# Kernel optimization log

Hardware: AMD Instinct MI355X
Metric: run time of the kernel (lower is better)

Reference implementation:

```python
import jax, jax.numpy as jnp
import numpy as np

N = 2048      # nodes
E = 65536     # edges (avg degree 32)
IN_C = 512
OUT_C = 512
KP1 = 3       # K=2 Chebyshev -> 3 terms


def setup_inputs() -> dict:
    key = jax.random.key(0)
    k0, k1, k2, k3, k4 = jax.random.split(key, 5)
    X_real = jax.random.normal(k0, (N, IN_C), jnp.float32)
    X_imag = jax.random.normal(k1, (N, IN_C), jnp.float32)
    edges = jax.random.randint(k2, (2, E), 0, N).astype(jnp.int64)
    edge_weight = jax.random.uniform(k3, (E,), jnp.float32)
    q = jnp.float32(0.25)
    stdv = 1.0 / np.sqrt(OUT_C)
    weight = jax.random.uniform(k4, (KP1, IN_C, OUT_C), jnp.float32, -stdv, stdv)
    bias = jnp.zeros((1, OUT_C), jnp.float32)
    return {"X_real": X_real, "X_imag": X_imag, "edges": edges, "q": q,
            "edge_weight": edge_weight, "weight": weight, "bias": bias}


def _cheb_laplacians(edges, edge_weight, q):
    """QinDirect_hermitian_decomp_sparse (norm=True, laplacian=True, max_eigen=2,
    gcn_appr=False) followed by cheb_poly_sparse with K=2. Returns stacked
    real/imag parts of [T0, T1, T2], each [KP1, N, N]."""
    f, e = edges[0], edges[1]
    A = jnp.zeros((N, N), jnp.float32).at[f, e].add(edge_weight)
    A_sym = 0.5 * (A + A.T)
    deg = A_sym.sum(axis=0)
    dinv = jnp.where(deg == 0.0, 1.0, deg) ** -0.5
    A_norm = dinv[:, None] * A_sym * dinv[None, :]   # D^-1/2 A_sym D^-1/2
    theta = (2.0 * jnp.pi) * q * (A - A.T)           # phase matrix
    # L = I - exp(i*theta) .* A_norm ; scaled (2/max_eigen)*L - I with max_eigen=2
    # => L_scaled = -exp(i*theta) .* A_norm
    L1_re = -jnp.cos(theta) * A_norm
    L1_im = -jnp.sin(theta) * A_norm
    eye = jnp.eye(N, dtype=jnp.float32)
    # T2 = 2*L1@L1 - I (complex square in real arithmetic)
    L2_re = 2.0 * (L1_re @ L1_re - L1_im @ L1_im) - eye
    L2_im = 2.0 * (L1_re @ L1_im + L1_im @ L1_re)
    L_re = jnp.stack([eye, L1_re, L2_re])                        # [KP1,N,N]
    L_im = jnp.stack([jnp.zeros((N, N), jnp.float32), L1_im, L2_im])
    return L_re, L_im


def reference(X_real, X_imag, edges, q, edge_weight, weight, bias):
    L_re, L_im = _cheb_laplacians(edges, edge_weight, q)
    # NOTE: original forward swaps the lists: L_norm_real = L_img, L_norm_imag = L_real.
    mr, mi = L_im, L_re
    # per term k: real_k = (mr_k@Xr - mi_k@Xi) @ W_k ; imag_k = (mi_k@Xr + mr_k@Xi) @ W_k
    Ar = jnp.einsum('knm,mf->knf', mr, X_real) - jnp.einsum('knm,mf->knf', mi, X_imag)
    Ai = jnp.einsum('knm,mf->knf', mi, X_real) + jnp.einsum('knm,mf->knf', mr, X_imag)
    real = jnp.einsum('knf,kfo->no', Ar, weight)   # sum over K terms
    imag = jnp.einsum('knf,kfo->no', Ai, weight)
    return real + bias, imag + bias
```

## Files before the change

### kernel.cpp

```cpp
#include <hip/hip_runtime.h>
#include <hip/hip_bf16.h>
#include <math.h>

#define NN 2048
#define CC 512
#define NEDGE 65536

typedef __hip_bfloat16 bf16;
typedef __attribute__((ext_vector_type(8))) short short8;
typedef __attribute__((ext_vector_type(4))) float floatx4;
typedef __attribute__((ext_vector_type(2))) float floatx2;
typedef __attribute__((ext_vector_type(4))) unsigned short us4;
typedef __attribute__((ext_vector_type(2))) unsigned short us2;

static constexpr float TWO_PI_F = 6.2831853071795864769f;

__device__ __forceinline__ unsigned short f2bu(float f) {
    bf16 h = __float2bfloat16(f);
    return *reinterpret_cast<unsigned short*>(&h);
}
__device__ __forceinline__ float bu2f(unsigned short u) {
    return __uint_as_float(((unsigned)u) << 16);
}
__device__ __forceinline__ int get_isbf(const void* qp) {
    return ((((const unsigned*)qp)[0] & 0xFFFFu) == 0x3E80u) ? 1 : 0;
}

__device__ __forceinline__ void gld16(const void* g, void* l) {
    __builtin_amdgcn_global_load_lds(
        (const __attribute__((address_space(1))) unsigned int*)(unsigned long long)(uintptr_t)g,
        (__attribute__((address_space(3))) unsigned int*)(unsigned long long)(uintptr_t)l,
        16, 0, 0);
}

__global__ __launch_bounds__(256) void prep_k(
    const void* __restrict__ xr, const void* __restrict__ xi,
    const void* __restrict__ edges, const void* __restrict__ qp,
    const void* __restrict__ ew, const void* __restrict__ Wt,
    int2* __restrict__ bucket, int* __restrict__ bcnt,
    bf16* __restrict__ Af, bf16* __restrict__ WTo, void* __restrict__ Xc)
{
    int bid = blockIdx.x, t = threadIdx.x;
    int isbf = get_isbf(qp);

    if (bid < 2048) {
        int r = bid;
        float fr0, fr1, fi0, fi1;
        if (isbf) {
            us2 vr = *(const us2*)((const bf16*)xr + (size_t)r * CC + 2 * t);
            us2 vi = *(const us2*)((const bf16*)xi + (size_t)r * CC + 2 * t);
            fr0 = bu2f(vr.x); fr1 = bu2f(vr.y); fi0 = bu2f(vi.x); fi1 = bu2f(vi.y);
        } else {
            floatx2 vr = *(const floatx2*)((const float*)xr + (size_t)r * CC + 2 * t);
            floatx2 vi = *(const floatx2*)((const float*)xi + (size_t)r * CC + 2 * t);
            fr0 = vr.x; fr1 = vr.y; fi0 = vi.x; fi1 = vi.y;
        }
        *(us2*)(Af + (size_t)r * 1536 + 2 * t)        = (us2){f2bu(-fi0), f2bu(-fi1)};
        *(us2*)(Af + (size_t)(NN + r) * 1536 + 2 * t) = (us2){f2bu(fr0), f2bu(fr1)};
        if (isbf)
            ((us4*)Xc)[(size_t)r * 256 + t] = (us4){f2bu(fr0), f2bu(fr1), f2bu(fi0), f2bu(fi1)};
        else
            ((floatx4*)Xc)[(size_t)r * 256 + t] = (floatx4){fr0, fr1, fi0, fi1};
    } else if (bid < 2816) {
        __shared__ float t1[32][33];
        int bw = bid - 2048;
        int k0 = (bw % 48) * 32, o0 = (bw / 48) * 32;
        int tx = t & 31, ty = t >> 5;
#pragma unroll
        for (int rr = 0; rr < 32; rr += 8) {
            size_t sidx = (size_t)(k0 + ty + rr) * CC + o0 + tx;
            t1[ty + rr][tx] = isbf ? __bfloat162float(((const bf16*)Wt)[sidx])
                                   : ((const float*)Wt)[sidx];
        }
        __syncthreads();
#pragma unroll
        for (int rr = 0; rr < 32; rr += 8)
            WTo[(size_t)(o0 + ty + rr) * 1536 + k0 + tx] = __float2bfloat16(t1[tx][ty + rr]);
    } else {
        __shared__ int s_i64;
        if (t < 64) {
            unsigned w0 = ((const unsigned*)edges)[2 * t + 1];
            unsigned w1 = ((const unsigned*)edges)[128 + 2 * t + 1];
            unsigned long long b = __ballot((w0 | w1) != 0u);
            if (t == 0) s_i64 = (b == 0ull) ? 1 : 0;
        }
        __syncthreads();
        int i64 = s_i64;
        int e = (bid - 2816) * 256 + t;
        int f, to;
        if (i64) {
            f  = (int)((const long long*)edges)[e];
            to = (int)((const long long*)edges)[NEDGE + e];
        } else {
            f  = ((const int*)edges)[e];
            to = ((const int*)edges)[NEDGE + e];
        }
        float wv = isbf ? __bfloat162float(((const bf16*)ew)[e]) : ((const float*)ew)[e];
        f &= (NN - 1); to &= (NN - 1);
        int wi = __float_as_int(wv);
        int s0 = atomicAdd(&bcnt[f], 1);
        if (s0 < 256) bucket[(size_t)f * 256 + s0] = make_int2(to, wi);
        int s1 = atomicAdd(&bcnt[to], 1);
        if (s1 < 256) bucket[(size_t)to * 256 + s1] = make_int2(f | 4096, wi);
    }
}

__global__ __launch_bounds__(256) void compact_k(
    const int2* __restrict__ bucket, const int* __restrict__ bcnt,
    float* __restrict__ dinv, int* __restrict__ ecol,
    floatx2* __restrict__ em, int* __restrict__ ecnt)
{
    __shared__ int      idx[NN];
    __shared__ unsigned pres[64];
    __shared__ int      pref[64];
    __shared__ float    s_s[256], s_d[256], red[256];
    __shared__ int      s_n;
    int i = blockIdx.x, t = threadIdx.x;

#pragma unroll
    for (int k = 0; k < NN / 256; ++k) idx[k * 256 + t] = -1;
    if (t < 64) pres[t] = 0u;
    s_s[t] = 0.f; s_d[t] = 0.f;
    __syncthreads();

    int cnt = bcnt[i]; if (cnt > 256) cnt = 256;
    int col = 0, dir = 0; float w = 0.f;
    if (t < cnt) {
        int2 e = bucket[(size_t)i * 256 + t];
        col = e.x & (NN - 1); dir = (e.x >> 12) & 1;
        w = __int_as_float(e.y);
    }
    red[t] = (t < cnt) ? w : 0.f;
    __syncthreads();
    for (int off = 128; off > 0; off >>= 1) {
        if (t < off) red[t] += red[t + off];
        __syncthreads();
    }
    if (t == 0) {
        float d = 0.5f * red[0];
        if (d == 0.f) d = 1.f;
        dinv[i] = rsqrtf(d);
    }
    if (t < cnt) atomicCAS(&idx[col], -1, t);
    __syncthreads();
    bool winner = (t < cnt) && (idx[col] == t);
    if (winner) atomicOr(&pres[col >> 5], 1u << (col & 31));
    __syncthreads();
    if (t == 0) {
        int run = 0;
        for (int wd = 0; wd < 64; ++wd) { pref[wd] = run; run += __popc(pres[wd]); }
        s_n = run;
        ecnt[i] = run;
    }
    __syncthreads();
    if (winner) {
        int slot = pref[col >> 5] + __popc(pres[col >> 5] & ((1u << (col & 31)) - 1u));
        idx[col] = slot;
        ecol[i * 256 + slot] = col;
    }
    __syncthreads();
    if (t < cnt) {
        int sl = idx[col];
        atomicAdd(&s_s[sl], w);
        atomicAdd(&s_d[sl], dir ? -w : w);
    }
    __syncthreads();
    if (t < s_n)
        em[i * 256 + t] = (floatx2){s_s[t], s_d[t]};
}

template<int EPI>
__global__ __launch_bounds__(256) void spmm_k(
    const int* __restrict__ ecol, const floatx2* __restrict__ em,
    const int* __restrict__ ecnt, const float* __restrict__ dinv,
    const void* __restrict__ qp,
    const void* __restrict__ xr, const void* __restrict__ xi,
    const void* __restrict__ Xc, const bf16* __restrict__ Z1in,
    bf16* __restrict__ Z1out, bf16* __restrict__ Af)
{
    int i = blockIdx.x, t = threadIdx.x;
    int isbf = get_isbf(qp);
    int n = ecnt[i];
    __shared__ int   sc[256];
    __shared__ float sre[256], sim[256];
    if (t < n) {
        float qv = isbf ? __bfloat162float(((const bf16*)qp)[0]) : ((const float*)qp)[0];
        int j = ecol[i * 256 + t];
        floatx2 sd = em[i * 256 + t];
        float an = dinv[i] * (0.5f * sd.x) * dinv[j];
        float th = TWO_PI_F * qv * sd.y;
        float sn, cs;
        sincosf(th, &sn, &cs);
        sc[t] = j; sre[t] = -cs * an; sim[t] = sn * an;
    }
    __syncthreads();
    float ar0 = 0.f, ar1 = 0.f, ai0 = 0.f, ai1 = 0.f;

    if (EPI == 1 && !isbf) {
        const floatx4* X4 = (const floatx4*)Xc;
#pragma unroll 4
        for (int s = 0; s < n; ++s) {
            int j = sc[s];
            float re = sre[s], im = sim[s];
            floatx4 v = X4[(((unsigned)j) << 8) + t];
            ar0 += re * v.x - im * v.z;  ai0 += re * v.z + im * v.x;
            ar1 += re * v.y - im * v.w;  ai1 += re * v.w + im * v.y;
        }
    } else {
        const us4* X4 = (const us4*)(EPI == 1 ? Xc : (const void*)Z1in);
#pragma unroll 4
        for (int s = 0; s < n; ++s) {
            int j = sc[s];
            float re = sre[s], im = sim[s];
            us4 v = X4[(((unsigned)j) << 8) + t];
            float vr0 = bu2f(v.x), vr1 = bu2f(v.y);
            float vi0 = bu2f(v.z), vi1 = bu2f(v.w);
            ar0 += re * vr0 - im * vi0;  ai0 += re * vi0 + im * vr0;
            ar1 += re * vr1 - im * vi1;  ai1 += re * vi1 + im * vr1;
        }
    }

    if (EPI == 1) {
        *(us4*)(Z1out + (size_t)i * 1024 + 4 * t) =
            (us4){f2bu(ar0), f2bu(ar1), f2bu(ai0), f2bu(ai1)};
        *(us2*)(Af + (size_t)i * 1536 + 512 + 2 * t)        = (us2){f2bu(-ai0), f2bu(-ai1)};
        *(us2*)(Af + (size_t)(NN + i) * 1536 + 512 + 2 * t) = (us2){f2bu(ar0), f2bu(ar1)};
    } else {
        float xr0, xr1, xi0, xi1;
        if (isbf) {
            us2 vr = *(const us2*)((const bf16*)xr + (size_t)i * CC + 2 * t);
            us2 vi = *(const us2*)((const bf16*)xi + (size_t)i * CC + 2 * t);
            xr0 = bu2f(vr.x); xr1 = bu2f(vr.y); xi0 = bu2f(vi.x); xi1 = bu2f(vi.y);
        } else {
            floatx2 vr = *(const floatx2*)((const float*)xr + (size_t)i * CC + 2 * t);
            floatx2 vi = *(const floatx2*)((const float*)xi + (size_t)i * CC + 2 * t);
            xr0 = vr.x; xr1 = vr.y; xi0 = vi.x; xi1 = vi.y;
        }
        float vre0 = 2.f * ar0 - xr0, vre1 = 2.f * ar1 - xr1;
        float vim0 = 2.f * ai0 - xi0, vim1 = 2.f * ai1 - xi1;
        *(us2*)(Af + (size_t)(NN + i) * 1536 + 1024 + 2 * t) = (us2){f2bu(vre0), f2bu(vre1)};
        *(us2*)(Af + (size_t)i * 1536 + 1024 + 2 * t)        = (us2){f2bu(-vim0), f2bu(-vim1)};
    }
}

__global__ void epi3_k(const bf16* __restrict__ Pb, const void* __restrict__ bias,
                       void* __restrict__ out, const void* __restrict__ qp) {
    int idx = blockIdx.x * 256 + threadIdx.x;
    if (idx >= 4096 * CC) return;
    int isbf = get_isbf(qp);
    int c = idx & (CC - 1);
    float s = 0.f;
#pragma unroll
    for (int z = 0; z < 4; ++z)
        s += __bfloat162float(Pb[(size_t)z * 4096 * CC + idx]);
    float bb = isbf ? __bfloat162float(((const bf16*)bias)[c]) : ((const float*)bias)[c];
    float o = s + bb;
    if (isbf) ((bf16*)out)[idx] = __float2bfloat16(o);
    else      ((float*)out)[idx] = o;
}

__global__ __launch_bounds__(256) void gemm_sk_k(
    const bf16* __restrict__ Ab, const bf16* __restrict__ BTb,
    int M, int N, int K, int klen,
    bf16* __restrict__ Pb)
{
    __shared__ bf16 sA[128 * 64];
    __shared__ bf16 sB[128 * 64];
    int tid = threadIdx.x;
    int w = tid >> 6, lane = tid & 63;
    int row0 = blockIdx.y * 128, col0 = blockIdx.x * 128;
    int kbase = blockIdx.z * klen;
    int wave_m = (w >> 1) * 64, wave_n = (w & 1) * 64;
    int lm = lane & 15, lq = lane >> 4;

    int srow = lane >> 3;
    int sg   = lane & 7;
    int scol = (sg ^ srow) * 8;
    const bf16 *gA[4], *gB[4];
    bf16 *lA[4], *lB[4];
#pragma unroll
    for (int i = 0; i < 4; ++i) {
        int c = w * 4 + i;
        int row = c * 8 + srow;
        gA[i] = Ab  + (size_t)(row0 + row) * K + kbase + scol;
        gB[i] = BTb + (size_t)(col0 + row) * K + kbase + scol;
        lA[i] = sA + c * 512 + lane * 8;
        lB[i] = sB + c * 512 + lane * 8;
    }

    floatx4 acc[4][4];
#pragma unroll
    for (int mf = 0; mf < 4; ++mf)
#pragma unroll
        for (int nf = 0; nf < 4; ++nf)
            acc[mf][nf] = (floatx4){0.f, 0.f, 0.f, 0.f};

    for (int kk = 0; kk < klen; kk += 64) {
        __syncthreads();
#pragma unroll
        for (int i = 0; i < 4; ++i) {
            gld16(gA[i] + kk, lA[i]);
            gld16(gB[i] + kk, lB[i]);
        }
        __syncthreads();
#pragma unroll
        for (int ks = 0; ks < 2; ++ks) {
            short8 af[4], bfv[4];
#pragma unroll
            for (int mf = 0; mf < 4; ++mf) {
                int row = wave_m + mf * 16 + lm;
                int g = (ks * 4 + lq) ^ (row & 7);
                af[mf] = *(const short8*)&sA[row * 64 + g * 8];
            }
#pragma unroll
            for (int nf = 0; nf < 4; ++nf) {
                int row = wave_n + nf * 16 + lm;
                int g = (ks * 4 + lq) ^ (row & 7);
                bfv[nf] = *(const short8*)&sB[row * 64 + g * 8];
            }
#pragma unroll
            for (int mf = 0; mf < 4; ++mf)
#pragma unroll
                for (int nf = 0; nf < 4; ++nf)
                    acc[mf][nf] = __builtin_amdgcn_mfma_f32_16x16x32_bf16(
                        af[mf], bfv[nf], acc[mf][nf], 0, 0, 0);
        }
    }

    bf16* slice = Pb + (size_t)blockIdx.z * M * N;
#pragma unroll
    for (int mf = 0; mf < 4; ++mf) {
#pragma unroll
        for (int nf = 0; nf < 4; ++nf) {
            int gcol = col0 + wave_n + nf * 16 + lm;
#pragma unroll
            for (int r = 0; r < 4; ++r) {
                int grow = row0 + wave_m + mf * 16 + lq * 4 + r;
                slice[(size_t)grow * N + gcol] = __float2bfloat16(acc[mf][nf][r]);
            }
        }
    }
}


extern "C" void kernel_launch(void* const* d_in, const int* in_sizes, int n_in,
                              void* d_out, int out_size, void* d_ws, size_t ws_size,
                              hipStream_t stream) {
    const void* Xr_in = d_in[0];
    const void* Xi_in = d_in[1];
    const void* edges = d_in[2];
    const void* q     = d_in[3];
    const void* ew    = d_in[4];
    const void* Wt    = d_in[5];
    const void* bias  = d_in[6];

    char* base = (char*)d_ws;
    const size_t MB = 1024 * 1024;
    int2*    bucket = (int2*)(base);
    int*     bcnt   = (int*)(base + 8 * MB);
    void*    Xc     = (void*)(base + 12 * MB);
    bf16*    Af     = (bf16*)(base + 32 * MB);
    bf16*    WT     = (bf16*)(base + 44 * MB);
    bf16*    Z1c    = (bf16*)(base + 46 * MB);
    float*   dinv   = (float*)(base + 54 * MB);
    int*     ecnt   = (int*)(base + 54 * MB + 16 * 1024);
    int*     ecol   = (int*)(base + 56 * MB);
    floatx2* em     = (floatx2*)(base + 58 * MB);
    bf16*    Pb     = (bf16*)(base + 56 * MB);

    hipMemsetAsync(bcnt, 0, NN * sizeof(int), stream);

    prep_k<<<3072, 256, 0, stream>>>(Xr_in, Xi_in, edges, q, ew, Wt,
                                     bucket, bcnt, Af, WT, Xc);
    compact_k<<<NN, 256, 0, stream>>>(bucket, bcnt, dinv, ecol, em, ecnt);

    spmm_k<1><<<NN, 256, 0, stream>>>(ecol, em, ecnt, dinv, q, Xr_in, Xi_in,
                                      Xc, nullptr, Z1c, Af);
    spmm_k<2><<<NN, 256, 0, stream>>>(ecol, em, ecnt, dinv, q, Xr_in, Xi_in,
                                      nullptr, Z1c, nullptr, Af);

    gemm_sk_k<<<dim3(CC / 128, 4096 / 128, 4), 256, 0, stream>>>(
        Af, WT, 4096, CC, 1536, 384, Pb);
    epi3_k<<<(4096 * CC) / 256, 256, 0, stream>>>(Pb, bias, d_out, q);
}
```

Before: 172.2 us.

## Regroup prep kernels, vectorize epilogue, raise spmm unroll and occupancy hint

Edge scattering moves into its own small kernel. Compaction is merged with the X and W conversion work into a single mid kernel that uses a shared-memory union, so the launch count stays the same but the grouping changes. The final reduction epilogue now handles four outputs per thread with vector loads and stores. The spmm kernel gets a launch_bounds occupancy hint and unroll 8 on its gather loop, which could raise register pressure or cause spills.

```diff
diff --git a/kernel.cpp b/kernel.cpp
--- a/kernel.cpp
+++ b/kernel.cpp
@@ -33,18 +33,116 @@
         16, 0, 0);
 }
 
-__global__ __launch_bounds__(256) void prep_k(
+__global__ __launch_bounds__(256) void scat_k(
+    const void* __restrict__ edges, const void* __restrict__ qp,
+    const void* __restrict__ ew,
+    int2* __restrict__ bucket, int* __restrict__ bcnt)
+{
+    __shared__ int s_i64;
+    int t = threadIdx.x;
+    int isbf = get_isbf(qp);
+    if (t < 64) {
+        unsigned w0 = ((const unsigned*)edges)[2 * t + 1];
+        unsigned w1 = ((const unsigned*)edges)[128 + 2 * t + 1];
+        unsigned long long b = __ballot((w0 | w1) != 0u);
+        if (t == 0) s_i64 = (b == 0ull) ? 1 : 0;
+    }
+    __syncthreads();
+    int i64 = s_i64;
+    int e = blockIdx.x * 256 + t;
+    int f, to;
+    if (i64) {
+        f  = (int)((const long long*)edges)[e];
+        to = (int)((const long long*)edges)[NEDGE + e];
+    } else {
+        f  = ((const int*)edges)[e];
+        to = ((const int*)edges)[NEDGE + e];
+    }
+    float wv = isbf ? __bfloat162float(((const bf16*)ew)[e]) : ((const float*)ew)[e];
+    f &= (NN - 1); to &= (NN - 1);
+    int wi = __float_as_int(wv);
+    int s0 = atomicAdd(&bcnt[f], 1);
+    if (s0 < 256) bucket[(size_t)f * 256 + s0] = make_int2(to, wi);
+    int s1 = atomicAdd(&bcnt[to], 1);
+    if (s1 < 256) bucket[(size_t)to * 256 + s1] = make_int2(f | 4096, wi);
+}
+
+__global__ __launch_bounds__(256) void mid_k(
+    const int2* __restrict__ bucket, const int* __restrict__ bcnt,
     const void* __restrict__ xr, const void* __restrict__ xi,
-    const void* __restrict__ edges, const void* __restrict__ qp,
-    const void* __restrict__ ew, const void* __restrict__ Wt,
-    int2* __restrict__ bucket, int* __restrict__ bcnt,
+    const void* __restrict__ qp, const void* __restrict__ Wt,
+    float* __restrict__ dinv, int* __restrict__ ecol,
+    floatx2* __restrict__ em, int* __restrict__ ecnt,
     bf16* __restrict__ Af, bf16* __restrict__ WTo, void* __restrict__ Xc)
 {
+    __shared__ union {
+        struct {
+            int      idx[NN];
+            unsigned pres[64];
+            int      pref[64];
+            float    s_s[256], s_d[256], red[256];
+            int      s_n;
+        } c;
+        float t1[32][33];
+    } sm;
     int bid = blockIdx.x, t = threadIdx.x;
     int isbf = get_isbf(qp);
 
     if (bid < 2048) {
-        int r = bid;
+        int i = bid;
+#pragma unroll
+        for (int k = 0; k < NN / 256; ++k) sm.c.idx[k * 256 + t] = -1;
+        if (t < 64) sm.c.pres[t] = 0u;
+        sm.c.s_s[t] = 0.f; sm.c.s_d[t] = 0.f;
+        __syncthreads();
+
+        int cnt = bcnt[i]; if (cnt > 256) cnt = 256;
+        int col = 0, dir = 0; float w = 0.f;
+        if (t < cnt) {
+            int2 e = bucket[(size_t)i * 256 + t];
+            col = e.x & (NN - 1); dir = (e.x >> 12) & 1;
+            w = __int_as_float(e.y);
+        }
+        sm.c.red[t] = (t < cnt) ? w : 0.f;
+        __syncthreads();
+        for (int off = 128; off > 0; off >>= 1) {
+            if (t < off) sm.c.red[t] += sm.c.red[t + off];
+            __syncthreads();
+        }
+        if (t == 0) {
+            float d = 0.5f * sm.c.red[0];
+            if (d == 0.f) d = 1.f;
+            dinv[i] = rsqrtf(d);
+        }
+        if (t < cnt) atomicCAS(&sm.c.idx[col], -1, t);
+        __syncthreads();
+        bool winner = (t < cnt) && (sm.c.idx[col] == t);
+        if (winner) atomicOr(&sm.c.pres[col >> 5], 1u << (col & 31));
+        __syncthreads();
+        if (t == 0) {
+            int run = 0;
+            for (int wd = 0; wd < 64; ++wd) { sm.c.pref[wd] = run; run += __popc(sm.c.pres[wd]); }
+            sm.c.s_n = run;
+            ecnt[i] = run;
+        }
+        __syncthreads();
+        if (winner) {
+            int slot = sm.c.pref[col >> 5] +
+                       __popc(sm.c.pres[col >> 5] & ((1u << (col & 31)) - 1u));
+            sm.c.idx[col] = slot;
+            ecol[i * 256 + slot] = col;
+        }
+        __syncthreads();
+        if (t < cnt) {
+            int sl = sm.c.idx[col];
+            atomicAdd(&sm.c.s_s[sl], w);
+            atomicAdd(&sm.c.s_d[sl], dir ? -w : w);
+        }
+        __syncthreads();
+        if (t < sm.c.s_n)
+            em[i * 256 + t] = (floatx2){sm.c.s_s[t], sm.c.s_d[t]};
+    } else if (bid < 4096) {
+        int r = bid - 2048;
         float fr0, fr1, fi0, fi1;
         if (isbf) {
             us2 vr = *(const us2*)((const bf16*)xr + (size_t)r * CC + 2 * t);
@@ -61,116 +159,25 @@
             ((us4*)Xc)[(size_t)r * 256 + t] = (us4){f2bu(fr0), f2bu(fr1), f2bu(fi0), f2bu(fi1)};
         else
             ((floatx4*)Xc)[(size_t)r * 256 + t] = (floatx4){fr0, fr1, fi0, fi1};
-    } else if (bid < 2816) {
-        __shared__ float t1[32][33];
-        int bw = bid - 2048;
+    } else {
+        int bw = bid - 4096;
         int k0 = (bw % 48) * 32, o0 = (bw / 48) * 32;
         int tx = t & 31, ty = t >> 5;
 #pragma unroll
         for (int rr = 0; rr < 32; rr += 8) {
             size_t sidx = (size_t)(k0 + ty + rr) * CC + o0 + tx;
-            t1[ty + rr][tx] = isbf ? __bfloat162float(((const bf16*)Wt)[sidx])
-                                   : ((const float*)Wt)[sidx];
+            sm.t1[ty + rr][tx] = isbf ? __bfloat162float(((const bf16*)Wt)[sidx])
+                                      : ((const float*)Wt)[sidx];
         }
         __syncthreads();
 #pragma unroll
         for (int rr = 0; rr < 32; rr += 8)
-            WTo[(size_t)(o0 + ty + rr) * 1536 + k0 + tx] = __float2bfloat16(t1[tx][ty + rr]);
-    } else {
-        __shared__ int s_i64;
-        if (t < 64) {
-            unsigned w0 = ((const unsigned*)edges)[2 * t + 1];
-            unsigned w1 = ((const unsigned*)edges)[128 + 2 * t + 1];
-            unsigned long long b = __ballot((w0 | w1) != 0u);
-            if (t == 0) s_i64 = (b == 0ull) ? 1 : 0;
-        }
-        __syncthreads();
-        int i64 = s_i64;
-        int e = (bid - 2816) * 256 + t;
-        int f, to;
-        if (i64) {
-            f  = (int)((const long long*)edges)[e];
-            to = (int)((const long long*)edges)[NEDGE + e];
-        } else {
-            f  = ((const int*)edges)[e];
-            to = ((const int*)edges)[NEDGE + e];
-        }
-        float wv = isbf ? __bfloat162float(((const bf16*)ew)[e]) : ((const float*)ew)[e];
-        f &= (NN - 1); to &= (NN - 1);
-        int wi = __float_as_int(wv);
-        int s0 = atomicAdd(&bcnt[f], 1);
-        if (s0 < 256) bucket[(size_t)f * 256 + s0] = make_int2(to, wi);
-        int s1 = atomicAdd(&bcnt[to], 1);
-        if (s1 < 256) bucket[(size_t)to * 256 + s1] = make_int2(f | 4096, wi);
-    }
-}
-
-__global__ __launch_bounds__(256) void compact_k(
-    const int2* __restrict__ bucket, const int* __restrict__ bcnt,
-    float* __restrict__ dinv, int* __restrict__ ecol,
-    floatx2* __restrict__ em, int* __restrict__ ecnt)
-{
-    __shared__ int      idx[NN];
-    __shared__ unsigned pres[64];
-    __shared__ int      pref[64];
-    __shared__ float    s_s[256], s_d[256], red[256];
-    __shared__ int      s_n;
-    int i = blockIdx.x, t = threadIdx.x;
-
-#pragma unroll
-    for (int k = 0; k < NN / 256; ++k) idx[k * 256 + t] = -1;
-    if (t < 64) pres[t] = 0u;
-    s_s[t] = 0.f; s_d[t] = 0.f;
-    __syncthreads();
-
-    int cnt = bcnt[i]; if (cnt > 256) cnt = 256;
-    int col = 0, dir = 0; float w = 0.f;
-    if (t < cnt) {
-        int2 e = bucket[(size_t)i * 256 + t];
-        col = e.x & (NN - 1); dir = (e.x >> 12) & 1;
-        w = __int_as_float(e.y);
-    }
-    red[t] = (t < cnt) ? w : 0.f;
-    __syncthreads();
-    for (int off = 128; off > 0; off >>= 1) {
-        if (t < off) red[t] += red[t + off];
-        __syncthreads();
-    }
-    if (t == 0) {
-        float d = 0.5f * red[0];
-        if (d == 0.f) d = 1.f;
-        dinv[i] = rsqrtf(d);
-    }
-    if (t < cnt) atomicCAS(&idx[col], -1, t);
-    __syncthreads();
-    bool winner = (t < cnt) && (idx[col] == t);
-    if (winner) atomicOr(&pres[col >> 5], 1u << (col & 31));
-    __syncthreads();
-    if (t == 0) {
-        int run = 0;
-        for (int wd = 0; wd < 64; ++wd) { pref[wd] = run; run += __popc(pres[wd]); }
-        s_n = run;
-        ecnt[i] = run;
-    }
-    __syncthreads();
-    if (winner) {
-        int slot = pref[col >> 5] + __popc(pres[col >> 5] & ((1u << (col & 31)) - 1u));
-        idx[col] = slot;
-        ecol[i * 256 + slot] = col;
-    }
-    __syncthreads();
-    if (t < cnt) {
-        int sl = idx[col];
-        atomicAdd(&s_s[sl], w);
-        atomicAdd(&s_d[sl], dir ? -w : w);
-    }
-    __syncthreads();
-    if (t < s_n)
-        em[i * 256 + t] = (floatx2){s_s[t], s_d[t]};
+            WTo[(size_t)(o0 + ty + rr) * 1536 + k0 + tx] = __float2bfloat16(sm.t1[tx][ty + rr]);
+    }
 }
 
 template<int EPI>
-__global__ __launch_bounds__(256) void spmm_k(
+__global__ __launch_bounds__(256, 8) void spmm_k(
     const int* __restrict__ ecol, const floatx2* __restrict__ em,
     const int* __restrict__ ecnt, const float* __restrict__ dinv,
     const void* __restrict__ qp,
@@ -198,7 +205,7 @@
 
     if (EPI == 1 && !isbf) {
         const floatx4* X4 = (const floatx4*)Xc;
-#pragma unroll 4
+#pragma unroll 8
         for (int s = 0; s < n; ++s) {
             int j = sc[s];
             float re = sre[s], im = sim[s];
@@ -208,7 +215,7 @@
         }
     } else {
         const us4* X4 = (const us4*)(EPI == 1 ? Xc : (const void*)Z1in);
-#pragma unroll 4
+#pragma unroll 8
         for (int s = 0; s < n; ++s) {
             int j = sc[s];
             float re = sre[s], im = sim[s];
@@ -243,20 +250,29 @@
     }
 }
 
-__global__ void epi3_k(const bf16* __restrict__ Pb, const void* __restrict__ bias,
-                       void* __restrict__ out, const void* __restrict__ qp) {
-    int idx = blockIdx.x * 256 + threadIdx.x;
-    if (idx >= 4096 * CC) return;
+__global__ __launch_bounds__(256) void epi3_k(
+    const bf16* __restrict__ Pb, const void* __restrict__ bias,
+    void* __restrict__ out, const void* __restrict__ qp)
+{
+    const int NG = 4096 * CC / 4;
+    int g = blockIdx.x * 256 + threadIdx.x;
+    if (g >= NG) return;
     int isbf = get_isbf(qp);
-    int c = idx & (CC - 1);
-    float s = 0.f;
-#pragma unroll
-    for (int z = 0; z < 4; ++z)
-        s += __bfloat162float(Pb[(size_t)z * 4096 * CC + idx]);
-    float bb = isbf ? __bfloat162float(((const bf16*)bias)[c]) : ((const float*)bias)[c];
-    float o = s + bb;
-    if (isbf) ((bf16*)out)[idx] = __float2bfloat16(o);
-    else      ((float*)out)[idx] = o;
+    int c4 = (g & 127) << 2;
+    float s0 = 0.f, s1 = 0.f, s2 = 0.f, s3 = 0.f;
+#pragma unroll
+    for (int z = 0; z < 4; ++z) {
+        us4 p = ((const us4*)Pb)[(size_t)z * NG + g];
+        s0 += bu2f(p.x); s1 += bu2f(p.y); s2 += bu2f(p.z); s3 += bu2f(p.w);
+    }
+    if (isbf) {
+        us4 bv = *(const us4*)((const bf16*)bias + c4);
+        ((us4*)out)[g] = (us4){f2bu(s0 + bu2f(bv.x)), f2bu(s1 + bu2f(bv.y)),
+                               f2bu(s2 + bu2f(bv.z)), f2bu(s3 + bu2f(bv.w))};
+    } else {
+        floatx4 bv = *(const floatx4*)((const float*)bias + c4);
+        ((floatx4*)out)[g] = (floatx4){s0 + bv.x, s1 + bv.y, s2 + bv.z, s3 + bv.w};
+    }
 }
 
 __global__ __launch_bounds__(256) void gemm_sk_k(
@@ -370,9 +386,10 @@
 
     hipMemsetAsync(bcnt, 0, NN * sizeof(int), stream);
 
-    prep_k<<<3072, 256, 0, stream>>>(Xr_in, Xi_in, edges, q, ew, Wt,
-                                     bucket, bcnt, Af, WT, Xc);
-    compact_k<<<NN, 256, 0, stream>>>(bucket, bcnt, dinv, ecol, em, ecnt);
+    scat_k<<<NEDGE / 256, 256, 0, stream>>>(edges, q, ew, bucket, bcnt);
+
+    mid_k<<<4864, 256, 0, stream>>>(bucket, bcnt, Xr_in, Xi_in, q, Wt,
+                                    dinv, ecol, em, ecnt, Af, WT, Xc);
 
     spmm_k<1><<<NN, 256, 0, stream>>>(ecol, em, ecnt, dinv, q, Xr_in, Xi_in,
                                       Xc, nullptr, Z1c, Af);
@@ -381,5 +398,5 @@
 
     gemm_sk_k<<<dim3(CC / 128, 4096 / 128, 4), 256, 0, stream>>>(
         Af, WT, 4096, CC, 1536, 384, Pb);
-    epi3_k<<<(4096 * CC) / 256, 256, 0, stream>>>(Pb, bias, d_out, q);
-}
+    epi3_k<<<(4096 * CC / 4) / 256, 256, 0, stream>>>(Pb, bias, d_out, q);
+}
```

New measurement: 178.0 us. 1.03x slower.
